# Kernel tuning notes

Measured on AMD Instinct MI355X. Metric: run time of the kernel, lower is better.

## Reference

```python
import jax, jax.numpy as jnp
import numpy as np

N = 50000      # nodes
E = 600000     # edges
G = 8          # graphs in the batch (for mean_nodes)
D = 128        # input_dim == hidden_dim
OUT = 10       # out_dim
NEG_SLOPE = 0.01  # nn.LeakyReLU default


def _lin(k, fi, fo):
    return jax.random.normal(k, (fi, fo), jnp.float32) / np.sqrt(fi).astype(np.float32)


def setup_inputs() -> dict:
    key = jax.random.key(0)
    ks = jax.random.split(key, 12)
    inputs = jax.random.normal(ks[0], (N, D), jnp.float32)
    src = jax.random.randint(ks[1], (E,), 0, N)
    dst = jax.random.randint(ks[2], (E,), 0, N)
    graph_id = jnp.sort(jax.random.randint(ks[3], (N,), 0, G))
    return {
        "inputs": inputs,
        "src": src,
        "dst": dst,
        "graph_id": graph_id,
        # GraphConv weights (DGL GraphConv: y = norm * A_norm x W + b)
        "W1": _lin(ks[4], D, D), "b1": jnp.zeros((D,), jnp.float32),
        "W2": _lin(ks[5], D, D), "b2": jnp.zeros((D,), jnp.float32),
        "W3": _lin(ks[6], D, D), "b3": jnp.zeros((D,), jnp.float32),
        # classifier head
        "Wc1": _lin(ks[7], D, 512),  "bc1": jnp.zeros((512,), jnp.float32),
        "Wc2": _lin(ks[8], 512, 256), "bc2": jnp.zeros((256,), jnp.float32),
        "Wc3": _lin(ks[9], 256, OUT), "bc3": jnp.zeros((OUT,), jnp.float32),
    }


def reference(inputs, src, dst, graph_id, W1, b1, W2, b2, W3, b3,
              Wc1, bc1, Wc2, bc2, Wc3, bc3):
    # DGL GraphConv with norm='both': h = D_in^{-1/2} A D_out^{-1/2} x W + b
    ones_e = jnp.ones((E,), jnp.float32)
    out_deg = jax.ops.segment_sum(ones_e, src, num_segments=N)
    in_deg = jax.ops.segment_sum(ones_e, dst, num_segments=N)
    src_norm = jnp.clip(out_deg, 1.0, None) ** -0.5   # [N]
    dst_norm = jnp.clip(in_deg, 1.0, None) ** -0.5    # [N]

    def gconv(x, W, b):
        x = x * src_norm[:, None]
        x = x @ W                                      # project first (in>=out)
        agg = jax.ops.segment_sum(x[src], dst, num_segments=N)  # SpMM
        return agg * dst_norm[:, None] + b

    h = gconv(inputs, W1, b1)
    h = gconv(h, W2, b2)
    h = gconv(h, W3, b3)

    # dgl.mean_nodes: per-graph mean over nodes
    sums = jax.ops.segment_sum(h, graph_id, num_segments=G)         # [G, D]
    cnts = jax.ops.segment_sum(jnp.ones((N,), jnp.float32), graph_id, num_segments=G)
    pooled = sums / jnp.clip(cnts, 1.0, None)[:, None]

    lrelu = lambda v: jax.nn.leaky_relu(v, NEG_SLOPE)
    x = lrelu(pooled @ Wc1 + bc1)
    x = lrelu(x @ Wc2 + bc2)
    x = lrelu(x @ Wc3 + bc3)
    return x
```

## Files before the change

kernel.cpp:

```cpp
#include <hip/hip_runtime.h>

#define Nn 50000
#define Ee 600000
#define Gg 8
#define Dd 128
#define NP 50048
#define NCHUNK 49

#define HWORDS 25024
#define HB 16
#define HIST_BLOCKS (2 * HB)
#define W12_BLOCKS 16
#define W123_BLOCKS 64
#define DTILE 64
#define DPBLK ((Nn + DTILE - 1) / DTILE)
#define RA_BLOCKS 128
#define RA_CHUNK ((DPBLK + RA_BLOCKS - 1) / RA_BLOCKS)

__global__ __launch_bounds__(1024) void hist_kernel(
    const int* __restrict__ src, const int* __restrict__ dst,
    unsigned int* __restrict__ phist,
    const float* __restrict__ W1, const float* __restrict__ W2,
    const float* __restrict__ W3, const float* __restrict__ b1,
    const float* __restrict__ b2,
    float* __restrict__ W12, float* __restrict__ e1, float* __restrict__ e2,
    int* __restrict__ accz)
{
    __shared__ unsigned int h[HWORDS];
    int t = threadIdx.x;
    int b = blockIdx.x;

    if (b < HIST_BLOCKS) {
        for (int i = t; i < HWORDS; i += 1024) h[i] = 0u;
        __syncthreads();
        int part = b >> 1;
        const int* arr = (b & 1) ? dst : src;
        int e0 = part * (Ee / HB);
        int eN = e0 + (Ee / HB);
        for (int e = e0 + t; e < eN; e += 1024) {
            int n = arr[e];
            atomicAdd(&h[n >> 1], 1u << ((n & 1) << 4));
        }
        __syncthreads();
        unsigned int* out = phist + (size_t)b * HWORDS;
        for (int i = t; i < HWORDS; i += 1024) out[i] = h[i];
    } else if (b < HIST_BLOCKS + W12_BLOCKS) {
        int j = (b - HIST_BLOCKS) * 8 + (t & 7);
        int k = t >> 3;
        float a = 0.f;
#pragma unroll 8
        for (int m = 0; m < 128; ++m) a += W1[k * 128 + m] * W2[m * 128 + j];
        W12[k * 128 + j] = a;
    } else {
        if (t < 128) {
            float a = 0.f;
#pragma unroll 8
            for (int k = 0; k < 128; ++k) a += b1[k] * W2[k * 128 + t];
            e1[t] = a;
        } else if (t < 256) {
            int c = t - 128;
            float a = 0.f;
#pragma unroll 8
            for (int k = 0; k < 128; ++k) a += b2[k] * W3[k * 128 + c];
            e2[c] = a;
        } else if (t < 256 + 88) {
            accz[t - 256] = 0;
        }
    }
}

__global__ __launch_bounds__(256) void scan_fused(
    const unsigned int* __restrict__ phist, const int* __restrict__ gid,
    float* __restrict__ srcn, float* __restrict__ pq, float* __restrict__ z,
    int* __restrict__ cnt, int* __restrict__ row_ptr, int* __restrict__ cursor,
    int* __restrict__ fs,
    const float* __restrict__ W12, const float* __restrict__ W3,
    const float* __restrict__ e1,
    float* __restrict__ W123, float* __restrict__ e1b)
{
    int b = blockIdx.x, t = threadIdx.x;
    if (b < NCHUNK) {
        __shared__ int tsum[256];
        __shared__ int lc[Gg];
        __shared__ int sbase;
        if (t < Gg) lc[t] = 0;
        __syncthreads();

        int d4[4];
        int wbase = b * 512 + t * 2;
#pragma unroll
        for (int wi = 0; wi < 2; ++wi) {
            int w = wbase + wi;
            unsigned so0 = 0, so1 = 0, si0 = 0, si1 = 0;
            if (w < HWORDS) {
#pragma unroll
                for (int p = 0; p < HB; ++p) {
                    unsigned a  = phist[(size_t)(2 * p) * HWORDS + w];
                    unsigned bb = phist[(size_t)(2 * p + 1) * HWORDS + w];
                    so0 += a & 0xffffu; so1 += a >> 16;
                    si0 += bb & 0xffffu; si1 += bb >> 16;
                }
            }
#pragma unroll
            for (int hh = 0; hh < 2; ++hh) {
                int n = 2 * w + hh;
                unsigned so = hh ? so1 : so0, si = hh ? si1 : si0;
                int d = 0;
                if (n < Nn) {
                    d = (int)so;
                    float sn = 1.f / sqrtf(fmaxf((float)so, 1.f));
                    float dn = 1.f / sqrtf(fmaxf((float)si, 1.f));
                    srcn[n] = sn; pq[n] = sn * dn;
                    int g = gid[n];
                    atomicAdd(&lc[g], 1);
                    float zr[8];
#pragma unroll
                    for (int gg = 0; gg < 8; ++gg) zr[gg] = (gg == g) ? dn : 0.f;
                    *(float4*)(z + (size_t)n * 8)     = *(float4*)zr;
                    *(float4*)(z + (size_t)n * 8 + 4) = *(float4*)(zr + 4);
                }
                d4[wi * 2 + hh] = d;
            }
        }
        int s = (d4[0] + d4[1]) + (d4[2] + d4[3]);
        tsum[t] = s;
        __syncthreads();
        for (int off = 1; off < 256; off <<= 1) {
            int x = (t >= off) ? tsum[t - off] : 0;
            __syncthreads();
            tsum[t] += x;
            __syncthreads();
        }
        int run = tsum[t] - s;

        if (t == 0) {
            int total = tsum[255];
            atomicExch(&fs[b], (total << 1) | 1);
            int base = 0;
            for (int p = 0; p < b; ++p) {
                int r;
                do { r = atomicAdd(&fs[p], 0); } while (!(r & 1));
                base += (r >> 1);
            }
            sbase = base;
        }
        __syncthreads();

        int gpos = sbase + run;
#pragma unroll
        for (int i = 0; i < 4; ++i) {
            int n = b * 1024 + t * 4 + i;
            if (n < Nn) { row_ptr[n] = gpos; cursor[n] = gpos; }
            gpos += d4[i];
        }
        if (b == NCHUNK - 1 && t == 255) row_ptr[Nn] = Ee;
        __syncthreads();
        if (t < Gg && lc[t] > 0) atomicAdd(&cnt[t], lc[t]);
    } else if (b < NCHUNK + W123_BLOCKS) {
        int j = (b - NCHUNK) * 2 + (t & 1);
        int k = t >> 1;
        float a = 0.f;
#pragma unroll 8
        for (int m = 0; m < 128; ++m) a += W12[k * 128 + m] * W3[m * 128 + j];
        W123[k * 128 + j] = a;
    } else {
        if (t < 128) {
            float a = 0.f;
#pragma unroll 8
            for (int k = 0; k < 128; ++k) a += e1[k] * W3[k * 128 + t];
            e1b[t] = a;
        }
    }
}

__global__ __launch_bounds__(256) void fill_kernel(
    const int* __restrict__ src, const int* __restrict__ dst,
    int* __restrict__ cursor, int* __restrict__ csr_dst)
{
    int e = blockIdx.x * 256 + threadIdx.x;
    if (e >= Ee) return;
    int pos = atomicAdd(&cursor[src[e]], 1);
    csr_dst[pos] = dst[e];
}

__global__ __launch_bounds__(256) void bspmm_kernel(
    const float* __restrict__ uin, const int* __restrict__ row_ptr,
    const int* __restrict__ csr, const float* __restrict__ scal,
    float* __restrict__ uout, const float* __restrict__ sn,
    float* __restrict__ pwout)
{
    int t = threadIdx.x;
    int m = blockIdx.x * 32 + (t >> 3);
    int g = t & 7;
    float acc = 0.f, snm = 0.f;
    if (m < Nn) {
        int beg = row_ptr[m], end = row_ptr[m + 1];
        int j = beg;
        if (scal) {
            float a0 = 0.f, a1 = 0.f, a2 = 0.f, a3 = 0.f;
            for (; j + 3 < end; j += 4) {
                int i0 = csr[j], i1 = csr[j + 1], i2 = csr[j + 2], i3 = csr[j + 3];
                float c0 = scal[i0], c1 = scal[i1], c2 = scal[i2], c3 = scal[i3];
                float u0 = uin[(size_t)i0 * 8 + g];
                float u1 = uin[(size_t)i1 * 8 + g];
                float u2 = uin[(size_t)i2 * 8 + g];
                float u3 = uin[(size_t)i3 * 8 + g];
                a0 += c0 * u0; a1 += c1 * u1; a2 += c2 * u2; a3 += c3 * u3;
            }
            for (; j < end; ++j) {
                int i0 = csr[j];
                a0 += scal[i0] * uin[(size_t)i0 * 8 + g];
            }
            acc = (a0 + a1) + (a2 + a3);
        } else {
            float a0 = 0.f, a1 = 0.f, a2 = 0.f, a3 = 0.f;
            for (; j + 3 < end; j += 4) {
                int i0 = csr[j], i1 = csr[j + 1], i2 = csr[j + 2], i3 = csr[j + 3];
                a0 += uin[(size_t)i0 * 8 + g];
                a1 += uin[(size_t)i1 * 8 + g];
                a2 += uin[(size_t)i2 * 8 + g];
                a3 += uin[(size_t)i3 * 8 + g];
            }
            for (; j < end; ++j) a0 += uin[(size_t)csr[j] * 8 + g];
            acc = (a0 + a1) + (a2 + a3);
        }
        uout[(size_t)m * 8 + g] = acc;
        if (pwout) snm = sn[m];
    }
    if (pwout) {
        __shared__ float red[Gg];
        if (t < Gg) red[t] = 0.f;
        __syncthreads();
        float v = snm * acc;
        v += __shfl_xor(v, 8, 64);
        v += __shfl_xor(v, 16, 64);
        v += __shfl_xor(v, 32, 64);
        if ((t & 63) < 8) atomicAdd(&red[t & 7], v);
        __syncthreads();
        if (t < Gg) atomicAdd(&pwout[t], red[t]);
    }
}

__global__ __launch_bounds__(256) void dotpool_kernel(
    const float* __restrict__ x, const float* __restrict__ u2,
    const float* __restrict__ pq, const float* __restrict__ sn,
    const int* __restrict__ row_ptr, const int* __restrict__ csr,
    float* __restrict__ partial)
{
    __shared__ float xs[DTILE][Dd];
    __shared__ float f[DTILE][Gg];
    int t = threadIdx.x;
    int n0 = blockIdx.x * DTILE;

    {
        const float4* x4 = (const float4*)x;
        float4* xs4 = (float4*)xs;
#pragma unroll
        for (int k = 0; k < 8; ++k) {
            int idx = t + 256 * k;
            int i = idx >> 5;
            int n = n0 + i;
            xs4[idx] = (n < Nn) ? x4[(size_t)n * 32 + (idx & 31)]
                                : make_float4(0.f, 0.f, 0.f, 0.f);
        }
    }

    {
        int i = t >> 2, sub = t & 3;
        int n = n0 + i;
        float ax = 0.f, ay = 0.f, s = 0.f;
        if (n < Nn) {
            s = sn[n];
            int beg = row_ptr[n], end = row_ptr[n + 1];
            int j = beg;
            float bx = 0.f, by = 0.f;
            for (; j + 1 < end; j += 2) {
                int i0 = csr[j], i1 = csr[j + 1];
                float c0 = pq[i0], c1 = pq[i1];
                float2 u0 = *(const float2*)(u2 + (size_t)i0 * 8 + sub * 2);
                float2 u1 = *(const float2*)(u2 + (size_t)i1 * 8 + sub * 2);
                ax += c0 * u0.x; ay += c0 * u0.y;
                bx += c1 * u1.x; by += c1 * u1.y;
            }
            if (j < end) {
                int i0 = csr[j];
                float c0 = pq[i0];
                float2 u = *(const float2*)(u2 + (size_t)i0 * 8 + sub * 2);
                ax += c0 * u.x; ay += c0 * u.y;
            }
            ax += bx; ay += by;
        }
        f[i][sub * 2 + 0] = s * ax;
        f[i][sub * 2 + 1] = s * ay;
    }
    __syncthreads();

    {
        int g = t >> 5, c = t & 31;
        float4 acc = {0.f, 0.f, 0.f, 0.f};
#pragma unroll 8
        for (int i = 0; i < DTILE; ++i) {
            float fv = f[i][g];
            float4 xv = *(const float4*)&xs[i][c * 4];
            acc.x += fv * xv.x; acc.y += fv * xv.y;
            acc.z += fv * xv.z; acc.w += fv * xv.w;
        }
        *(float4*)(partial + (size_t)blockIdx.x * 1024 + g * 128 + c * 4) = acc;
    }
}

__global__ __launch_bounds__(256) void dotreduceA_kernel(
    const float* __restrict__ partial, float* __restrict__ partial2)
{
    int b = blockIdx.x, t = threadIdx.x;
    int p0 = b * RA_CHUNK;
    int p1 = p0 + RA_CHUNK; if (p1 > DPBLK) p1 = DPBLK;
    float a0 = 0.f, a1 = 0.f, a2 = 0.f, a3 = 0.f;
    for (int p = p0; p < p1; ++p) {
        const float* pp = partial + (size_t)p * 1024;
        a0 += pp[t];
        a1 += pp[t + 256];
        a2 += pp[t + 512];
        a3 += pp[t + 768];
    }
    float* o = partial2 + (size_t)b * 1024;
    o[t] = a0; o[t + 256] = a1; o[t + 512] = a2; o[t + 768] = a3;
}

__global__ __launch_bounds__(256) void redx0_kernel(
    const float* __restrict__ partial2, const float* __restrict__ pw1r,
    const float* __restrict__ pw2r, const int* __restrict__ cnt,
    const float* __restrict__ W123, const float* __restrict__ e1b,
    const float* __restrict__ e2, const float* __restrict__ b3,
    float* __restrict__ x0g)
{
    __shared__ float ps[256];
    int t = threadIdx.x;
    int o = blockIdx.x * 256 + t;
    float a0 = 0.f, a1 = 0.f, a2 = 0.f, a3 = 0.f;
#pragma unroll 4
    for (int b = 0; b < RA_BLOCKS; b += 4) {
        a0 += partial2[(size_t)(b + 0) * 1024 + o];
        a1 += partial2[(size_t)(b + 1) * 1024 + o];
        a2 += partial2[(size_t)(b + 2) * 1024 + o];
        a3 += partial2[(size_t)(b + 3) * 1024 + o];
    }
    ps[t] = (a0 + a1) + (a2 + a3);
    __syncthreads();

    int g = o >> 7, c = o & 127, gl = t >> 7;
    float a = 0.f;
#pragma unroll 8
    for (int k = 0; k < 128; ++k) a += ps[gl * 128 + k] * W123[k * 128 + c];
    float inv = 1.f / fmaxf((float)cnt[g], 1.f);
    x0g[o] = a * inv + (pw2r[g] * inv) * e1b[c] + (pw1r[g] * inv) * e2[c] + b3[c];
}

__global__ __launch_bounds__(256) void fc1_kernel(
    const float* __restrict__ x0g, const float* __restrict__ Wc1,
    const float* __restrict__ bc1, float* __restrict__ x1g)
{
    __shared__ float xs[Gg * 128];
    __shared__ float par[256];
    int t = threadIdx.x;
    for (int i = t; i < Gg * 128; i += 256) xs[i] = x0g[i];
    __syncthreads();
    int h = t >> 7, rem = t & 127;
    int g = rem >> 4, m = blockIdx.x * 16 + (rem & 15);
    int k0 = h * 64;
    float a = 0.f;
#pragma unroll 16
    for (int k = 0; k < 64; ++k) a += xs[g * 128 + k0 + k] * Wc1[(size_t)(k0 + k) * 512 + m];
    par[t] = a;
    __syncthreads();
    if (t < 128) {
        float v = par[t] + par[t + 128] + bc1[m];
        x1g[g * 512 + m] = v > 0.f ? v : 0.01f * v;
    }
}

__global__ __launch_bounds__(256) void fc2_kernel(
    const float* __restrict__ x1g, const float* __restrict__ Wc2,
    const float* __restrict__ bc2, float* __restrict__ x2g)
{
    __shared__ float xs[Gg * 512];
    __shared__ float par[256];
    int t = threadIdx.x;
    for (int i = t; i < Gg * 512; i += 256) xs[i] = x1g[i];
    __syncthreads();
    int q = t >> 6, rem = t & 63;
    int g = rem >> 3, m = blockIdx.x * 8 + (rem & 7);
    int k0 = q * 128;
    float a = 0.f;
#pragma unroll 16
    for (int k = 0; k < 128; ++k) a += xs[g * 512 + k0 + k] * Wc2[(size_t)(k0 + k) * 256 + m];
    par[t] = a;
    __syncthreads();
    if (t < 64) {
        float v = par[t] + par[t + 64] + par[t + 128] + par[t + 192] + bc2[m];
        x2g[g * 256 + m] = v > 0.f ? v : 0.01f * v;
    }
}

__global__ __launch_bounds__(640) void fc3_kernel(
    const float* __restrict__ x2g, const float* __restrict__ Wc3,
    const float* __restrict__ bc3, float* __restrict__ out)
{
    __shared__ float xs[Gg * 256];
    int t = threadIdx.x;
    for (int i = t; i < Gg * 256; i += 640) xs[i] = x2g[i];
    __syncthreads();
    int w = t >> 6, lane = t & 63;
    if (w < 10) {
        float acc[Gg];
#pragma unroll
        for (int g = 0; g < Gg; ++g) acc[g] = 0.f;
#pragma unroll
        for (int kk = 0; kk < 4; ++kk) {
            int k = lane + kk * 64;
            float wv = Wc3[(size_t)k * 10 + w];
#pragma unroll
            for (int g = 0; g < Gg; ++g) acc[g] += xs[g * 256 + k] * wv;
        }
#pragma unroll
        for (int g = 0; g < Gg; ++g) {
            float v = acc[g];
            for (int off = 32; off; off >>= 1) v += __shfl_down(v, off, 64);
            if (lane == 0) {
                v += bc3[w];
                out[g * 10 + w] = v > 0.f ? v : 0.01f * v;
            }
        }
    }
}

extern "C" void kernel_launch(void* const* d_in, const int* in_sizes, int n_in,
                              void* d_out, int out_size, void* d_ws, size_t ws_size,
                              hipStream_t stream)
{
    const float* inputs = (const float*)d_in[0];
    const int*   src    = (const int*)d_in[1];
    const int*   dst    = (const int*)d_in[2];
    const int*   gid    = (const int*)d_in[3];
    const float* W1  = (const float*)d_in[4];
    const float* b1  = (const float*)d_in[5];
    const float* W2  = (const float*)d_in[6];
    const float* b2  = (const float*)d_in[7];
    const float* W3  = (const float*)d_in[8];
    const float* b3  = (const float*)d_in[9];
    const float* Wc1 = (const float*)d_in[10];
    const float* bc1 = (const float*)d_in[11];
    const float* Wc2 = (const float*)d_in[12];
    const float* bc2 = (const float*)d_in[13];
    const float* Wc3 = (const float*)d_in[14];
    const float* bc3 = (const float*)d_in[15];

    int*   wi      = (int*)d_ws;
    int*   row_ptr = wi;
    int*   cursor  = row_ptr + NP;
    int*   csr_dst = cursor + NP;
    float* wf      = (float*)(csr_dst + Ee);
    float* srcn    = wf;
    float* pq      = srcn + NP;
    float* z       = pq + NP;
    float* u1      = z + (size_t)NP * 8;
    float* u2      = u1 + (size_t)NP * 8;
    float* partial = u2 + (size_t)NP * 8;
    float* partial2= partial + (size_t)DPBLK * 1024;
    float* pw1     = partial2 + (size_t)RA_BLOCKS * 1024;
    float* pw2     = pw1 + Gg;
    int*   cnt     = (int*)(pw2 + Gg);
    int*   fs      = cnt + Gg;
    float* W12v    = (float*)(fs + 64);
    float* W123v   = W12v + 128 * 128;
    float* e1v     = W123v + 128 * 128;
    float* e1bv    = e1v + 128;
    float* e2v     = e1bv + 128;
    float* x0g     = e2v + 128;
    float* x1g     = x0g + 1024;
    float* x2g     = x1g + 4096;
    unsigned int* phist = (unsigned int*)(x2g + 2048);

    hist_kernel<<<HIST_BLOCKS + W12_BLOCKS + 1, 1024, 0, stream>>>(
        src, dst, phist, W1, W2, W3, b1, b2, W12v, e1v, e2v, (int*)pw1);
    scan_fused<<<NCHUNK + W123_BLOCKS + 1, 256, 0, stream>>>(
        phist, gid, srcn, pq, z, cnt, row_ptr, cursor, fs,
        W12v, W3, e1v, W123v, e1bv);
    fill_kernel<<<(Ee + 255) / 256, 256, 0, stream>>>(src, dst, cursor, csr_dst);

    int bblocks = (Nn + 31) / 32;
    bspmm_kernel<<<bblocks, 256, 0, stream>>>(z, row_ptr, csr_dst, nullptr,
                                              u1, srcn, pw1);
    bspmm_kernel<<<bblocks, 256, 0, stream>>>(u1, row_ptr, csr_dst, pq,
                                              u2, srcn, pw2);

    dotpool_kernel<<<DPBLK, 256, 0, stream>>>(inputs, u2, pq, srcn,
                                              row_ptr, csr_dst, partial);
    dotreduceA_kernel<<<RA_BLOCKS, 256, 0, stream>>>(partial, partial2);
    redx0_kernel<<<4, 256, 0, stream>>>(partial2, pw1, pw2, cnt,
                                        W123v, e1bv, e2v, b3, x0g);
    fc1_kernel<<<32, 256, 0, stream>>>(x0g, Wc1, bc1, x1g);
    fc2_kernel<<<32, 256, 0, stream>>>(x1g, Wc2, bc2, x2g);
    fc3_kernel<<<1, 640, 0, stream>>>(x2g, Wc3, bc3, (float*)d_out);
}
```

Measured before the change: 176.5 us.

## Fuse classifier head into one grid-synced kernel and push pq scaling into SpMM output

```diff
diff --git a/kernel.cpp b/kernel.cpp
--- a/kernel.cpp
+++ b/kernel.cpp
@@ -16,6 +16,7 @@
 #define DPBLK ((Nn + DTILE - 1) / DTILE)
 #define RA_BLOCKS 128
 #define RA_CHUNK ((DPBLK + RA_BLOCKS - 1) / RA_BLOCKS)
+#define HEAD_BLOCKS 32
 
 __global__ __launch_bounds__(1024) void hist_kernel(
     const int* __restrict__ src, const int* __restrict__ dst,
@@ -63,7 +64,7 @@
 #pragma unroll 8
             for (int k = 0; k < 128; ++k) a += b2[k] * W3[k * 128 + c];
             e2[c] = a;
-        } else if (t < 256 + 88) {
+        } else if (t < 256 + 96) {
             accz[t - 256] = 0;
         }
     }
@@ -185,46 +186,35 @@
 
 __global__ __launch_bounds__(256) void bspmm_kernel(
     const float* __restrict__ uin, const int* __restrict__ row_ptr,
-    const int* __restrict__ csr, const float* __restrict__ scal,
+    const int* __restrict__ csr, const float* __restrict__ pqv,
     float* __restrict__ uout, const float* __restrict__ sn,
     float* __restrict__ pwout)
 {
     int t = threadIdx.x;
+    int g = t & 7;
     int m = blockIdx.x * 32 + (t >> 3);
-    int g = t & 7;
     float acc = 0.f, snm = 0.f;
     if (m < Nn) {
         int beg = row_ptr[m], end = row_ptr[m + 1];
         int j = beg;
-        if (scal) {
-            float a0 = 0.f, a1 = 0.f, a2 = 0.f, a3 = 0.f;
-            for (; j + 3 < end; j += 4) {
-                int i0 = csr[j], i1 = csr[j + 1], i2 = csr[j + 2], i3 = csr[j + 3];
-                float c0 = scal[i0], c1 = scal[i1], c2 = scal[i2], c3 = scal[i3];
-                float u0 = uin[(size_t)i0 * 8 + g];
-                float u1 = uin[(size_t)i1 * 8 + g];
-                float u2 = uin[(size_t)i2 * 8 + g];
-                float u3 = uin[(size_t)i3 * 8 + g];
-                a0 += c0 * u0; a1 += c1 * u1; a2 += c2 * u2; a3 += c3 * u3;
-            }
-            for (; j < end; ++j) {
-                int i0 = csr[j];
-                a0 += scal[i0] * uin[(size_t)i0 * 8 + g];
-            }
-            acc = (a0 + a1) + (a2 + a3);
-        } else {
-            float a0 = 0.f, a1 = 0.f, a2 = 0.f, a3 = 0.f;
-            for (; j + 3 < end; j += 4) {
-                int i0 = csr[j], i1 = csr[j + 1], i2 = csr[j + 2], i3 = csr[j + 3];
-                a0 += uin[(size_t)i0 * 8 + g];
-                a1 += uin[(size_t)i1 * 8 + g];
-                a2 += uin[(size_t)i2 * 8 + g];
-                a3 += uin[(size_t)i3 * 8 + g];
-            }
-            for (; j < end; ++j) a0 += uin[(size_t)csr[j] * 8 + g];
-            acc = (a0 + a1) + (a2 + a3);
-        }
-        uout[(size_t)m * 8 + g] = acc;
+        float a0 = 0.f, a1 = 0.f, a2 = 0.f, a3 = 0.f;
+        float a4 = 0.f, a5 = 0.f, a6 = 0.f, a7 = 0.f;
+        for (; j + 7 < end; j += 8) {
+            int i0 = csr[j],     i1 = csr[j + 1], i2 = csr[j + 2], i3 = csr[j + 3];
+            int i4 = csr[j + 4], i5 = csr[j + 5], i6 = csr[j + 6], i7 = csr[j + 7];
+            a0 += uin[(size_t)i0 * 8 + g]; a1 += uin[(size_t)i1 * 8 + g];
+            a2 += uin[(size_t)i2 * 8 + g]; a3 += uin[(size_t)i3 * 8 + g];
+            a4 += uin[(size_t)i4 * 8 + g]; a5 += uin[(size_t)i5 * 8 + g];
+            a6 += uin[(size_t)i6 * 8 + g]; a7 += uin[(size_t)i7 * 8 + g];
+        }
+        for (; j + 3 < end; j += 4) {
+            int i0 = csr[j], i1 = csr[j + 1], i2 = csr[j + 2], i3 = csr[j + 3];
+            a0 += uin[(size_t)i0 * 8 + g]; a1 += uin[(size_t)i1 * 8 + g];
+            a2 += uin[(size_t)i2 * 8 + g]; a3 += uin[(size_t)i3 * 8 + g];
+        }
+        for (; j < end; ++j) a0 += uin[(size_t)csr[j] * 8 + g];
+        acc = ((a0 + a1) + (a2 + a3)) + ((a4 + a5) + (a6 + a7));
+        uout[(size_t)m * 8 + g] = pqv[m] * acc;
         if (pwout) snm = sn[m];
     }
     if (pwout) {
@@ -242,8 +232,8 @@
 }
 
 __global__ __launch_bounds__(256) void dotpool_kernel(
-    const float* __restrict__ x, const float* __restrict__ u2,
-    const float* __restrict__ pq, const float* __restrict__ sn,
+    const float* __restrict__ x, const float* __restrict__ u2p,
+    const float* __restrict__ sn,
     const int* __restrict__ row_ptr, const int* __restrict__ csr,
     float* __restrict__ partial)
 {
@@ -273,22 +263,21 @@
             s = sn[n];
             int beg = row_ptr[n], end = row_ptr[n + 1];
             int j = beg;
-            float bx = 0.f, by = 0.f;
-            for (; j + 1 < end; j += 2) {
-                int i0 = csr[j], i1 = csr[j + 1];
-                float c0 = pq[i0], c1 = pq[i1];
-                float2 u0 = *(const float2*)(u2 + (size_t)i0 * 8 + sub * 2);
-                float2 u1 = *(const float2*)(u2 + (size_t)i1 * 8 + sub * 2);
-                ax += c0 * u0.x; ay += c0 * u0.y;
-                bx += c1 * u1.x; by += c1 * u1.y;
+            float bx = 0.f, by = 0.f, cx = 0.f, cy = 0.f, dx = 0.f, dy = 0.f;
+            for (; j + 3 < end; j += 4) {
+                int i0 = csr[j], i1 = csr[j + 1], i2 = csr[j + 2], i3 = csr[j + 3];
+                float2 u0 = *(const float2*)(u2p + (size_t)i0 * 8 + sub * 2);
+                float2 u1 = *(const float2*)(u2p + (size_t)i1 * 8 + sub * 2);
+                float2 u2 = *(const float2*)(u2p + (size_t)i2 * 8 + sub * 2);
+                float2 u3 = *(const float2*)(u2p + (size_t)i3 * 8 + sub * 2);
+                ax += u0.x; ay += u0.y; bx += u1.x; by += u1.y;
+                cx += u2.x; cy += u2.y; dx += u3.x; dy += u3.y;
             }
-            if (j < end) {
-                int i0 = csr[j];
-                float c0 = pq[i0];
-                float2 u = *(const float2*)(u2 + (size_t)i0 * 8 + sub * 2);
-                ax += c0 * u.x; ay += c0 * u.y;
+            for (; j < end; ++j) {
+                float2 u = *(const float2*)(u2p + (size_t)csr[j] * 8 + sub * 2);
+                ax += u.x; ay += u.y;
             }
-            ax += bx; ay += by;
+            ax += bx + cx + dx; ay += by + cy + dy;
         }
         f[i][sub * 2 + 0] = s * ax;
         f[i][sub * 2 + 1] = s * ay;
@@ -327,109 +316,141 @@
     o[t] = a0; o[t + 256] = a1; o[t + 512] = a2; o[t + 768] = a3;
 }
 
-__global__ __launch_bounds__(256) void redx0_kernel(
+__device__ __forceinline__ void gsync(int* ctr, int t)
+{
+    __threadfence();
+    __syncthreads();
+    if (t == 0) {
+        atomicAdd(ctr, 1);
+        while (atomicAdd(ctr, 0) < HEAD_BLOCKS) {}
+    }
+    __syncthreads();
+    __threadfence();
+}
+
+__global__ __launch_bounds__(256) void head_kernel(
     const float* __restrict__ partial2, const float* __restrict__ pw1r,
     const float* __restrict__ pw2r, const int* __restrict__ cnt,
     const float* __restrict__ W123, const float* __restrict__ e1b,
     const float* __restrict__ e2, const float* __restrict__ b3,
-    float* __restrict__ x0g)
-{
-    __shared__ float ps[256];
-    int t = threadIdx.x;
-    int o = blockIdx.x * 256 + t;
-    float a0 = 0.f, a1 = 0.f, a2 = 0.f, a3 = 0.f;
+    const float* __restrict__ Wc1, const float* __restrict__ bc1,
+    const float* __restrict__ Wc2, const float* __restrict__ bc2,
+    const float* __restrict__ Wc3, const float* __restrict__ bc3,
+    float* __restrict__ pooled, float* __restrict__ x0g,
+    float* __restrict__ x1g, float* __restrict__ x2g,
+    int* __restrict__ done, float* __restrict__ out)
+{
+    __shared__ float shm[4352];
+    int b = blockIdx.x, t = threadIdx.x;
+
+    {
+        float* red = shm;
+        int ol = t & 31, q = t >> 5;
+        int o = b * 32 + ol;
+        float a = 0.f;
+        int p0 = q * 16;
 #pragma unroll 4
-    for (int b = 0; b < RA_BLOCKS; b += 4) {
-        a0 += partial2[(size_t)(b + 0) * 1024 + o];
-        a1 += partial2[(size_t)(b + 1) * 1024 + o];
-        a2 += partial2[(size_t)(b + 2) * 1024 + o];
-        a3 += partial2[(size_t)(b + 3) * 1024 + o];
-    }
-    ps[t] = (a0 + a1) + (a2 + a3);
-    __syncthreads();
-
-    int g = o >> 7, c = o & 127, gl = t >> 7;
-    float a = 0.f;
-#pragma unroll 8
-    for (int k = 0; k < 128; ++k) a += ps[gl * 128 + k] * W123[k * 128 + c];
-    float inv = 1.f / fmaxf((float)cnt[g], 1.f);
-    x0g[o] = a * inv + (pw2r[g] * inv) * e1b[c] + (pw1r[g] * inv) * e2[c] + b3[c];
-}
-
-__global__ __launch_bounds__(256) void fc1_kernel(
-    const float* __restrict__ x0g, const float* __restrict__ Wc1,
-    const float* __restrict__ bc1, float* __restrict__ x1g)
-{
-    __shared__ float xs[Gg * 128];
-    __shared__ float par[256];
-    int t = threadIdx.x;
-    for (int i = t; i < Gg * 128; i += 256) xs[i] = x0g[i];
-    __syncthreads();
-    int h = t >> 7, rem = t & 127;
-    int g = rem >> 4, m = blockIdx.x * 16 + (rem & 15);
-    int k0 = h * 64;
-    float a = 0.f;
+        for (int p = p0; p < p0 + 16; ++p)
+            a += partial2[(size_t)p * 1024 + o];
+        red[ol * 8 + q] = a;
+        __syncthreads();
+        if (t < 32) {
+            float s = 0.f;
+#pragma unroll
+            for (int q2 = 0; q2 < 8; ++q2) s += red[t * 8 + q2];
+            pooled[b * 32 + t] = s;
+        }
+    }
+    gsync(&done[0], t);
+
+    {
+        float* prow = shm;
+        float* red  = shm + 128;
+        int g = (b * 32) >> 7;
+        if (t < 128) prow[t] = pooled[g * 128 + t];
+        __syncthreads();
+        int ol = t & 31, q = t >> 5;
+        int o = b * 32 + ol, c = o & 127;
+        float a = 0.f;
+        int k0 = q * 16;
+#pragma unroll 4
+        for (int k = k0; k < k0 + 16; ++k)
+            a += prow[k] * W123[k * 128 + c];
+        red[ol * 8 + q] = a;
+        __syncthreads();
+        if (t < 32) {
+            int oo = b * 32 + t, cc = oo & 127;
+            float s = 0.f;
+#pragma unroll
+            for (int q2 = 0; q2 < 8; ++q2) s += red[t * 8 + q2];
+            float inv = 1.f / fmaxf((float)cnt[g], 1.f);
+            x0g[oo] = s * inv + (pw2r[g] * inv) * e1b[cc]
+                    + (pw1r[g] * inv) * e2[cc] + b3[cc];
+        }
+    }
+    gsync(&done[1], t);
+
+    {
+        float* xs  = shm;
+        float* par = shm + 1024;
+        for (int i = t; i < 1024; i += 256) xs[i] = x0g[i];
+        __syncthreads();
+        int h = t >> 7, rem = t & 127;
+        int g = rem >> 4, m = b * 16 + (rem & 15);
+        int k0 = h * 64;
+        float a = 0.f;
 #pragma unroll 16
-    for (int k = 0; k < 64; ++k) a += xs[g * 128 + k0 + k] * Wc1[(size_t)(k0 + k) * 512 + m];
-    par[t] = a;
-    __syncthreads();
-    if (t < 128) {
-        float v = par[t] + par[t + 128] + bc1[m];
-        x1g[g * 512 + m] = v > 0.f ? v : 0.01f * v;
-    }
-}
-
-__global__ __launch_bounds__(256) void fc2_kernel(
-    const float* __restrict__ x1g, const float* __restrict__ Wc2,
-    const float* __restrict__ bc2, float* __restrict__ x2g)
-{
-    __shared__ float xs[Gg * 512];
-    __shared__ float par[256];
-    int t = threadIdx.x;
-    for (int i = t; i < Gg * 512; i += 256) xs[i] = x1g[i];
-    __syncthreads();
-    int q = t >> 6, rem = t & 63;
-    int g = rem >> 3, m = blockIdx.x * 8 + (rem & 7);
-    int k0 = q * 128;
-    float a = 0.f;
+        for (int k = 0; k < 64; ++k)
+            a += xs[g * 128 + k0 + k] * Wc1[(size_t)(k0 + k) * 512 + m];
+        par[t] = a;
+        __syncthreads();
+        if (t < 128) {
+            int g2 = t >> 4, m2 = b * 16 + (t & 15);
+            float v = par[t] + par[t + 128] + bc1[m2];
+            x1g[g2 * 512 + m2] = v > 0.f ? v : 0.01f * v;
+        }
+    }
+    gsync(&done[2], t);
+
+    {
+        float* xs  = shm;
+        float* par = shm + 4096;
+        for (int i = t; i < 4096; i += 256) xs[i] = x1g[i];
+        __syncthreads();
+        int q = t >> 6, rem = t & 63;
+        int g = rem >> 3, m = b * 8 + (rem & 7);
+        int k0 = q * 128;
+        float a = 0.f;
 #pragma unroll 16
-    for (int k = 0; k < 128; ++k) a += xs[g * 512 + k0 + k] * Wc2[(size_t)(k0 + k) * 256 + m];
-    par[t] = a;
-    __syncthreads();
-    if (t < 64) {
-        float v = par[t] + par[t + 64] + par[t + 128] + par[t + 192] + bc2[m];
-        x2g[g * 256 + m] = v > 0.f ? v : 0.01f * v;
-    }
-}
-
-__global__ __launch_bounds__(640) void fc3_kernel(
-    const float* __restrict__ x2g, const float* __restrict__ Wc3,
-    const float* __restrict__ bc3, float* __restrict__ out)
-{
-    __shared__ float xs[Gg * 256];
-    int t = threadIdx.x;
-    for (int i = t; i < Gg * 256; i += 640) xs[i] = x2g[i];
-    __syncthreads();
-    int w = t >> 6, lane = t & 63;
-    if (w < 10) {
-        float acc[Gg];
-#pragma unroll
-        for (int g = 0; g < Gg; ++g) acc[g] = 0.f;
-#pragma unroll
-        for (int kk = 0; kk < 4; ++kk) {
-            int k = lane + kk * 64;
-            float wv = Wc3[(size_t)k * 10 + w];
-#pragma unroll
-            for (int g = 0; g < Gg; ++g) acc[g] += xs[g * 256 + k] * wv;
-        }
-#pragma unroll
-        for (int g = 0; g < Gg; ++g) {
-            float v = acc[g];
-            for (int off = 32; off; off >>= 1) v += __shfl_down(v, off, 64);
-            if (lane == 0) {
-                v += bc3[w];
-                out[g * 10 + w] = v > 0.f ? v : 0.01f * v;
+        for (int k = 0; k < 128; ++k)
+            a += xs[g * 512 + k0 + k] * Wc2[(size_t)(k0 + k) * 256 + m];
+        par[t] = a;
+        __syncthreads();
+        if (t < 64) {
+            int g2 = t >> 3, m2 = b * 8 + (t & 7);
+            float v = par[t] + par[t + 64] + par[t + 128] + par[t + 192] + bc2[m2];
+            x2g[g2 * 256 + m2] = v > 0.f ? v : 0.01f * v;
+        }
+    }
+    gsync(&done[3], t);
+    if (b != 0) return;
+
+    {
+        float* xs = shm;
+        for (int i = t; i < 2048; i += 256) xs[i] = x2g[i];
+        __syncthreads();
+        if (t < 80) {
+            int g = t / 10, w = t - g * 10;
+            const float* xr = xs + g * 256;
+            float a0 = 0.f, a1 = 0.f, a2 = 0.f, a3 = 0.f;
+            for (int k = 0; k < 256; k += 4) {
+                a0 += xr[k + 0] * Wc3[(size_t)(k + 0) * 10 + w];
+                a1 += xr[k + 1] * Wc3[(size_t)(k + 1) * 10 + w];
+                a2 += xr[k + 2] * Wc3[(size_t)(k + 2) * 10 + w];
+                a3 += xr[k + 3] * Wc3[(size_t)(k + 3) * 10 + w];
             }
+            float v = (a0 + a1) + (a2 + a3) + bc3[w];
+            out[g * 10 + w] = v > 0.f ? v : 0.01f * v;
         }
     }
 }
@@ -471,7 +492,8 @@
     float* pw2     = pw1 + Gg;
     int*   cnt     = (int*)(pw2 + Gg);
     int*   fs      = cnt + Gg;
-    float* W12v    = (float*)(fs + 64);
+    int*   done    = fs + 64;
+    float* W12v    = (float*)(done + 8);
     float* W123v   = W12v + 128 * 128;
     float* e1v     = W123v + 128 * 128;
     float* e1bv    = e1v + 128;
@@ -479,7 +501,8 @@
     float* x0g     = e2v + 128;
     float* x1g     = x0g + 1024;
     float* x2g     = x1g + 4096;
-    unsigned int* phist = (unsigned int*)(x2g + 2048);
+    float* pooledv = x2g + 2048;
+    unsigned int* phist = (unsigned int*)(pooledv + 1024);
 
     hist_kernel<<<HIST_BLOCKS + W12_BLOCKS + 1, 1024, 0, stream>>>(
         src, dst, phist, W1, W2, W3, b1, b2, W12v, e1v, e2v, (int*)pw1);
@@ -489,17 +512,16 @@
     fill_kernel<<<(Ee + 255) / 256, 256, 0, stream>>>(src, dst, cursor, csr_dst);
 
     int bblocks = (Nn + 31) / 32;
-    bspmm_kernel<<<bblocks, 256, 0, stream>>>(z, row_ptr, csr_dst, nullptr,
+    bspmm_kernel<<<bblocks, 256, 0, stream>>>(z, row_ptr, csr_dst, pq,
                                               u1, srcn, pw1);
     bspmm_kernel<<<bblocks, 256, 0, stream>>>(u1, row_ptr, csr_dst, pq,
                                               u2, srcn, pw2);
 
-    dotpool_kernel<<<DPBLK, 256, 0, stream>>>(inputs, u2, pq, srcn,
+    dotpool_kernel<<<DPBLK, 256, 0, stream>>>(inputs, u2, srcn,
                                               row_ptr, csr_dst, partial);
     dotreduceA_kernel<<<RA_BLOCKS, 256, 0, stream>>>(partial, partial2);
-    redx0_kernel<<<4, 256, 0, stream>>>(partial2, pw1, pw2, cnt,
-                                        W123v, e1bv, e2v, b3, x0g);
-    fc1_kernel<<<32, 256, 0, stream>>>(x0g, Wc1, bc1, x1g);
-    fc2_kernel<<<32, 256, 0, stream>>>(x1g, Wc2, bc2, x2g);
-    fc3_kernel<<<1, 640, 0, stream>>>(x2g, Wc3, bc3, (float*)d_out);
-}
+    head_kernel<<<HEAD_BLOCKS, 256, 0, stream>>>(
+        partial2, pw1, pw2, cnt, W123v, e1bv, e2v, b3,
+        Wc1, bc1, Wc2, bc2, Wc3, bc3,
+        pooledv, x0g, x1g, x2g, done, (float*)d_out);
+}
```

Result: no change. 177.8 us (+0.8%).
